# Performance work log

Hardware: AMD Instinct MI355X
Metric: run time of the kernel (lower is better)

Reference implementation:

```python
import jax, jax.numpy as jnp
import numpy as np

DIM = 768
HID = 3072
HID2 = HID // 2
MAX_LEVEL = 8
N_LEV = MAX_LEVEL + 1
BATCH, SEQ = 2, 2048
EPS = 1e-5


def _layernorm(x, gamma, beta):
    m = jnp.mean(x, axis=-1, keepdims=True)
    v = jnp.mean(jnp.square(x - m), axis=-1, keepdims=True)
    return (x - m) * jax.lax.rsqrt(v + EPS) * gamma + beta


def setup_inputs() -> dict:
    key = jax.random.key(0)
    ks = jax.random.split(key, 12)
    s = 0.02
    return {
        "x": jax.random.normal(ks[0], (BATCH, SEQ, DIM), dtype=jnp.float32),
        "levels_info": jax.random.randint(ks[1], (SEQ, 4), 0, N_LEV, dtype=jnp.int32),
        "gamma": jnp.ones((DIM,), dtype=jnp.float32),
        "beta": jnp.zeros((DIM,), dtype=jnp.float32),
        "W1": jax.random.normal(ks[2], (DIM, HID), dtype=jnp.float32) * s,
        "b1": jnp.zeros((HID,), dtype=jnp.float32),
        "W2": jax.random.normal(ks[3], (HID, DIM), dtype=jnp.float32) * s,
        "b2": jnp.zeros((DIM,), dtype=jnp.float32),
        "A1": jax.random.normal(ks[4], (N_LEV, DIM, HID2), dtype=jnp.float32) * s,
        "a1b": jnp.zeros((N_LEV, HID2), dtype=jnp.float32),
        "A2": jax.random.normal(ks[5], (N_LEV, HID2, DIM), dtype=jnp.float32) * s,
        "a2b": jnp.zeros((N_LEV, DIM), dtype=jnp.float32),
        "lmw": jnp.ones((N_LEV,), dtype=jnp.float32)
        + jax.random.normal(ks[6], (N_LEV,), dtype=jnp.float32) * 0.1,
    }


def reference(x, levels_info, gamma, beta, W1, b1, W2, b2, A1, a1b, A2, a2b, lmw):
    # x: [B,S,D]
    x_norm = _layernorm(x, gamma, beta)
    # main MLP: Linear -> GELU (exact, torch default) -> Linear; dropout=0 is identity
    h = jax.nn.gelu(jnp.einsum("bsd,dh->bsh", x_norm, W1) + b1, approximate=False)
    main_out = jnp.einsum("bsh,hd->bsd", h, W2) + b2

    # per-token depth-indexed adapter routing
    depths = jnp.clip(levels_info[:, 0], 0, MAX_LEVEL)  # [S]
    level_adapted = jnp.zeros_like(main_out)
    for lvl in range(N_LEV):  # small fixed expert set
        mask = (depths == lvl).astype(x.dtype)[None, :, None]  # [1,S,1]
        hl = jax.nn.relu(jnp.einsum("bsd,dh->bsh", x_norm, A1[lvl]) + a1b[lvl])
        level_adapted = level_adapted + mask * (
            jnp.einsum("bsh,hd->bsd", hl, A2[lvl]) + a2b[lvl]
        )

    # softmax over the sequence axis (faithful to F.softmax(..., dim=0))
    mix = jax.nn.softmax(lmw[depths], axis=0)[None, :, None]  # [1,S,1]
    return main_out * (1.0 - mix) + level_adapted * mix
```

## Files before the change

kernel.cpp:

```cpp
#include <hip/hip_runtime.h>
#include <hip/hip_bf16.h>
#include <math.h>

typedef __bf16 bf16;
typedef __bf16 bf16x4 __attribute__((ext_vector_type(4)));
typedef __bf16 bf16x8 __attribute__((ext_vector_type(8)));
typedef float f32x4 __attribute__((ext_vector_type(4)));

#define DIM 768
#define HID 3072
#define HID2 1536
#define NLEV 9
#define SEQ 2048
#define ROWS 4096
#define MAXPAD 5248
#define MAXTILES 41

__device__ __forceinline__ void gld16(const void* g, void* l) {
    __builtin_amdgcn_global_load_lds(
        (const __attribute__((address_space(1))) void*)g,
        (__attribute__((address_space(3))) void*)l, 16, 0, 0);
}


__device__ __forceinline__ void ln_body(int row, float* sm,
                                        const float* __restrict__ x,
                                        const float* __restrict__ gamma,
                                        const float* __restrict__ beta,
                                        bf16* __restrict__ xn) {
    int tid = threadIdx.x;
    const float* xr = x + (size_t)row * DIM;
    float v0 = xr[tid], v1 = xr[tid + 256], v2 = xr[tid + 512];
    float s = v0 + v1 + v2;
    float q = v0 * v0 + v1 * v1 + v2 * v2;
    for (int off = 32; off; off >>= 1) {
        s += __shfl_down(s, off, 64);
        q += __shfl_down(q, off, 64);
    }
    int wv = tid >> 6, ln = tid & 63;
    if (ln == 0) { sm[wv] = s; sm[4 + wv] = q; }
    __syncthreads();
    if (tid == 0) {
        float S = sm[0] + sm[1] + sm[2] + sm[3];
        float Q = sm[4] + sm[5] + sm[6] + sm[7];
        float m = S * (1.0f / DIM);
        float var = Q * (1.0f / DIM) - m * m;
        sm[8] = m;
        sm[9] = rsqrtf(var + 1e-5f);
    }
    __syncthreads();
    float m = sm[8], r = sm[9];
    bf16* xo = xn + (size_t)row * DIM;
    xo[tid]       = (bf16)((v0 - m) * r * gamma[tid]       + beta[tid]);
    xo[tid + 256] = (bf16)((v1 - m) * r * gamma[tid + 256] + beta[tid + 256]);
    xo[tid + 512] = (bf16)((v2 - m) * r * gamma[tid + 512] + beta[tid + 512]);
}

__device__ __forceinline__ void transpose_body(float* sm,
                                               const float* __restrict__ inb,
                                               bf16* __restrict__ outb,
                                               int R, int C, int bx, int by) {
    float (*tile)[33] = (float (*)[33])sm;
    int tx = threadIdx.x & 31, ty = threadIdx.x >> 5;
#pragma unroll
    for (int i = 0; i < 4; i++) {
        int r = by * 32 + ty + i * 8;
        tile[ty + i * 8][tx] = inb[(size_t)r * C + bx * 32 + tx];
    }
    __syncthreads();
#pragma unroll
    for (int i = 0; i < 4; i++) {
        int c = bx * 32 + ty + i * 8;
        outb[(size_t)c * R + by * 32 + tx] = (bf16)tile[tx][ty + i * 8];
    }
}

__device__ __forceinline__ void routing_body(float* sm,
                                             const int* __restrict__ levels_info,
                                             const float* __restrict__ lmw,
                                             float* __restrict__ mix,
                                             int* __restrict__ row_index,
                                             int* __restrict__ tile_meta,
                                             float* __restrict__ zbuf) {
    int* cnt = (int*)sm;
    int* cur = cnt + NLEV;
    int* off = cur + NLEV;
    float* mixv = (float*)(off + NLEV);
    int tid = threadIdx.x;
    if (tid < NLEV) { cnt[tid] = 0; cur[tid] = 0; }
    __syncthreads();
    for (int s = tid; s < SEQ; s += 256) {
        int d = levels_info[s * 4];
        d = d < 0 ? 0 : (d > 8 ? 8 : d);
        atomicAdd(&cnt[d], 1);
    }
    for (int i = tid; i < MAXPAD; i += 256) row_index[i] = -1;
    if (tid < 16) zbuf[tid] = 0.0f;
    __syncthreads();
    if (tid == 0) {
        float mx = lmw[0];
        for (int l = 1; l < NLEV; l++) mx = fmaxf(mx, lmw[l]);
        float denom = 0.f;
        for (int l = 0; l < NLEV; l++) denom += (float)cnt[l] * expf(lmw[l] - mx);
        float inv = 1.0f / denom;
        int running = 0, t = 0;
        for (int l = 0; l < NLEV; l++) {
            mixv[l] = expf(lmw[l] - mx) * inv;
            off[l] = running;
            int seg = (2 * cnt[l] + 127) & ~127;
            for (int k = 0; k < seg / 128; k++) tile_meta[t++] = l;
            running += seg;
        }
        for (; t < MAXTILES; t++) tile_meta[t] = -1;
    }
    __syncthreads();
    for (int s = tid; s < SEQ; s += 256) {
        int d = levels_info[s * 4];
        d = d < 0 ? 0 : (d > 8 ? 8 : d);
        int p = atomicAdd(&cur[d], 2);
        row_index[off[d] + p]     = s;
        row_index[off[d] + p + 1] = s + SEQ;
        mix[s] = mixv[d];
    }
}

__global__ __launch_bounds__(256) void prep_kernel(const float* __restrict__ x,
                                                   const int* __restrict__ levels_info,
                                                   const float* __restrict__ gamma,
                                                   const float* __restrict__ beta,
                                                   const float* __restrict__ W1,
                                                   const float* __restrict__ W2,
                                                   const float* __restrict__ A1,
                                                   const float* __restrict__ A2,
                                                   const float* __restrict__ lmw,
                                                   bf16* __restrict__ Xn,
                                                   bf16* __restrict__ W1t,
                                                   bf16* __restrict__ W2t,
                                                   bf16* __restrict__ A1t,
                                                   bf16* __restrict__ A2t,
                                                   float* __restrict__ mix,
                                                   int* __restrict__ row_index,
                                                   int* __restrict__ tile_meta,
                                                   float* __restrict__ zbuf) {
    __shared__ __align__(16) float sm[32 * 33];
    int bid = blockIdx.x;
    if (bid == 0) { routing_body(sm, levels_info, lmw, mix, row_index, tile_meta, zbuf); return; }
    bid -= 1;
    if (bid < ROWS) { ln_body(bid, sm, x, gamma, beta, Xn); return; }
    bid -= ROWS;
    if (bid < 2304) {
        transpose_body(sm, W1, W1t, DIM, HID, bid % 96, bid / 96);
        return;
    }
    bid -= 2304;
    if (bid < 2304) {
        transpose_body(sm, W2, W2t, HID, DIM, bid % 24, bid / 24);
        return;
    }
    bid -= 2304;
    if (bid < 10368) {
        int bz = bid / 1152, r = bid % 1152;
        transpose_body(sm, A1 + (size_t)bz * DIM * HID2, A1t + (size_t)bz * DIM * HID2,
                       DIM, HID2, r % 48, r / 48);
        return;
    }
    bid -= 10368;
    {
        int bz = bid / 1152, r = bid % 1152;
        transpose_body(sm, A2 + (size_t)bz * HID2 * DIM, A2t + (size_t)bz * HID2 * DIM,
                       HID2, DIM, r % 24, r / 24);
    }
}

__device__ __forceinline__ void gemm_loop_db(const bf16* ga0, const bf16* ga1,
                                             int stepa0, int stepa1,
                                             const bf16* gb0, const bf16* gb1, int stepb,
                                             bf16* As, bf16* Bs,
                                             f32x4 (&acc)[4][4], int ktiles) {
    int tid = threadIdx.x;
    int wv = tid >> 6;
    int lane = tid & 63;
    int wm = wv >> 1, wn = wv & 1;
    int aoff = ((wm * 64) + (lane & 15)) * 32 + (lane >> 4) * 8;
    int boff = ((wn * 64) + (lane & 15)) * 32 + (lane >> 4) * 8;
    gld16(ga0, As + wv * 512);
    gld16(ga1, As + 2048 + wv * 512);
    gld16(gb0, Bs + wv * 512);
    gld16(gb1, Bs + 2048 + wv * 512);
    ga0 += stepa0; ga1 += stepa1; gb0 += stepb; gb1 += stepb;
    for (int kt = 0; kt < ktiles; ++kt) {
        __syncthreads();
        int cur = (kt & 1) << 12;
        int nxt = cur ^ 4096;
        if (kt + 1 < ktiles) {
            gld16(ga0, As + nxt + wv * 512);
            gld16(ga1, As + nxt + 2048 + wv * 512);
            gld16(gb0, Bs + nxt + wv * 512);
            gld16(gb1, Bs + nxt + 2048 + wv * 512);
            ga0 += stepa0; ga1 += stepa1; gb0 += stepb; gb1 += stepb;
        }
        bf16x8 af[4], bfr[4];
#pragma unroll
        for (int i = 0; i < 4; i++) af[i] = *(const bf16x8*)(As + cur + aoff + i * 512);
#pragma unroll
        for (int j = 0; j < 4; j++) bfr[j] = *(const bf16x8*)(Bs + cur + boff + j * 512);
#pragma unroll
        for (int i = 0; i < 4; i++)
#pragma unroll
            for (int j = 0; j < 4; j++)
                acc[i][j] = __builtin_amdgcn_mfma_f32_16x16x32_bf16(af[i], bfr[j], acc[i][j], 0, 0, 0);
    }
}

#define ACC_INIT(acc) \
    _Pragma("unroll") for (int i = 0; i < 4; i++) \
    _Pragma("unroll") for (int j = 0; j < 4; j++) acc[i][j] = (f32x4){0.f, 0.f, 0.f, 0.f};

__global__ __launch_bounds__(256) void mlp1_kernel(const bf16* __restrict__ Xn,
                                                   const bf16* __restrict__ W1t,
                                                   const float* __restrict__ b1,
                                                   bf16* __restrict__ H,
                                                   const bf16* __restrict__ A1t,
                                                   const float* __restrict__ a1b,
                                                   const int* __restrict__ row_index,
                                                   const int* __restrict__ tile_meta,
                                                   const bf16* __restrict__ zbuf,
                                                   bf16* __restrict__ HL) {
    __shared__ __align__(16) bf16 As[8192], Bs[8192];
    int bid = blockIdx.x, tid = threadIdx.x;
    int r0 = tid >> 2, cg = tid & 3;
    int lane = tid & 63, wv = tid >> 6, wm = wv >> 1, wn = wv & 1;
    f32x4 acc[4][4];
    ACC_INIT(acc);

    if (bid < 768) {
        int mb = bid & 31, nb = bid >> 5;
        const bf16* ga0 = Xn + (size_t)(mb * 128 + r0) * DIM + cg * 8;
        const bf16* ga1 = ga0 + (size_t)64 * DIM;
        const bf16* gb0 = W1t + (size_t)(nb * 128 + r0) * DIM + cg * 8;
        const bf16* gb1 = gb0 + (size_t)64 * DIM;
        gemm_loop_db(ga0, ga1, 32, 32, gb0, gb1, 32, As, Bs, acc, DIM / 32);
        int rbase = mb * 128 + wm * 64 + ((lane >> 4) << 2);
        int cbase = nb * 128 + wn * 64 + (lane & 15);
#pragma unroll
        for (int j = 0; j < 4; j++) {
            int c = cbase + j * 16;
            float bias = b1[c];
#pragma unroll
            for (int i = 0; i < 4; i++)
#pragma unroll
                for (int r = 0; r < 4; r++) {
                    int row = rbase + i * 16 + r;
                    float v = acc[i][j][r] + bias;
                    float g = 0.5f * v * (1.0f + erff(v * 0.70710678118f));
                    H[(size_t)row * HID + c] = (bf16)g;
                }
        }
    } else {
        int t2 = bid - 768;
        int t = t2 % MAXTILES, nb = t2 / MAXTILES;
        int lvl = tile_meta[t];
        if (lvl < 0) return;
        int ridx0 = row_index[t * 128 + r0];
        int ridx1 = row_index[t * 128 + 64 + r0];
        const bf16* ga0 = (ridx0 >= 0) ? (Xn + (size_t)ridx0 * DIM + cg * 8) : zbuf;
        const bf16* ga1 = (ridx1 >= 0) ? (Xn + (size_t)ridx1 * DIM + cg * 8) : zbuf;
        int sa0 = (ridx0 >= 0) ? 32 : 0;
        int sa1 = (ridx1 >= 0) ? 32 : 0;
        const bf16* Bl = A1t + (size_t)lvl * HID2 * DIM;
        const bf16* gb0 = Bl + (size_t)(nb * 128 + r0) * DIM + cg * 8;
        const bf16* gb1 = gb0 + (size_t)64 * DIM;
        gemm_loop_db(ga0, ga1, sa0, sa1, gb0, gb1, 32, As, Bs, acc, DIM / 32);
        int rbase = wm * 64 + ((lane >> 4) << 2);
        int cbase = nb * 128 + wn * 64 + (lane & 15);
#pragma unroll
        for (int j = 0; j < 4; j++) {
            int c = cbase + j * 16;
            float bias = a1b[lvl * HID2 + c];
#pragma unroll
            for (int i = 0; i < 4; i++)
#pragma unroll
                for (int r = 0; r < 4; r++) {
                    int rl = rbase + i * 16 + r;
                    float v = acc[i][j][r] + bias;
                    HL[(size_t)(t * 128 + rl) * HID2 + c] = (bf16)fmaxf(v, 0.0f);
                }
        }
    }
}

__global__ __launch_bounds__(256) void mlp2_kernel(const bf16* __restrict__ H,
                                                   const bf16* __restrict__ W2t,
                                                   bf16* __restrict__ part,
                                                   const bf16* __restrict__ HL,
                                                   const bf16* __restrict__ A2t,
                                                   const float* __restrict__ a2b,
                                                   const int* __restrict__ row_index,
                                                   const int* __restrict__ tile_meta,
                                                   bf16* __restrict__ apart) {
    __shared__ __align__(16) bf16 As[8192], Bs[8192];
    int bid = blockIdx.x, tid = threadIdx.x;
    int r0 = tid >> 2, cg = tid & 3;
    int lane = tid & 63, wv = tid >> 6, wm = wv >> 1, wn = wv & 1;
    f32x4 acc[4][4];
    ACC_INIT(acc);

    if (bid < 384) {
        int mb = bid & 31;
        int rest = bid >> 5;
        int nb = rest % 6;
        int ks = rest / 6;
        const bf16* ga0 = H + (size_t)(mb * 128 + r0) * HID + ks * 1536 + cg * 8;
        const bf16* ga1 = ga0 + (size_t)64 * HID;
        const bf16* gb0 = W2t + (size_t)(nb * 128 + r0) * HID + ks * 1536 + cg * 8;
        const bf16* gb1 = gb0 + (size_t)64 * HID;
        gemm_loop_db(ga0, ga1, 32, 32, gb0, gb1, 32, As, Bs, acc, 48);
        bf16* pk = part + (size_t)ks * ROWS * DIM;
        int rbase = mb * 128 + wm * 64 + ((lane >> 4) << 2);
        int cbase = nb * 128 + wn * 64 + (lane & 15);
#pragma unroll
        for (int j = 0; j < 4; j++) {
            int c = cbase + j * 16;
#pragma unroll
            for (int i = 0; i < 4; i++)
#pragma unroll
                for (int r = 0; r < 4; r++) {
                    int row = rbase + i * 16 + r;
                    pk[(size_t)row * DIM + c] = (bf16)acc[i][j][r];
                }
        }
    } else {
        int t2 = bid - 384;
        int t = t2 % MAXTILES, nb = t2 / MAXTILES;
        int lvl = tile_meta[t];
        if (lvl < 0) return;
        const bf16* ga0 = HL + (size_t)(t * 128 + r0) * HID2 + cg * 8;
        const bf16* ga1 = ga0 + (size_t)64 * HID2;
        const bf16* Bl = A2t + (size_t)lvl * DIM * HID2;
        const bf16* gb0 = Bl + (size_t)(nb * 128 + r0) * HID2 + cg * 8;
        const bf16* gb1 = gb0 + (size_t)64 * HID2;
        gemm_loop_db(ga0, ga1, 32, 32, gb0, gb1, 32, As, Bs, acc, HID2 / 32);
        int rbase = wm * 64 + ((lane >> 4) << 2);
        int cbase = nb * 128 + wn * 64 + (lane & 15);
#pragma unroll
        for (int i = 0; i < 4; i++)
#pragma unroll
            for (int r = 0; r < 4; r++) {
                int rl = rbase + i * 16 + r;
                int rg = row_index[t * 128 + rl];
                if (rg >= 0) {
#pragma unroll
                    for (int j = 0; j < 4; j++) {
                        int c = cbase + j * 16;
                        apart[(size_t)rg * DIM + c] = (bf16)(acc[i][j][r] + a2b[lvl * DIM + c]);
                    }
                }
            }
    }
}

__global__ __launch_bounds__(256) void combine_kernel(const bf16* __restrict__ part,
                                                      const bf16* __restrict__ apart,
                                                      const float* __restrict__ b2,
                                                      const float* __restrict__ mix,
                                                      float* __restrict__ out) {
    int i = blockIdx.x * 256 + threadIdx.x;
    int base = i * 4;
    int row = base / DIM;
    int c = base - row * DIM;
    float mx = mix[row & (SEQ - 1)];
    bf16x4 p0 = *(const bf16x4*)(part + base);
    bf16x4 p1 = *(const bf16x4*)(part + (size_t)ROWS * DIM + base);
    bf16x4 ap = *(const bf16x4*)(apart + base);
    float4 o;
    float* po = &o.x;
#pragma unroll
    for (int k = 0; k < 4; k++) {
        float main_v = (float)p0[k] + (float)p1[k] + b2[c + k];
        po[k] = (1.0f - mx) * main_v + mx * (float)ap[k];
    }
    *(float4*)(out + base) = o;
}

extern "C" void kernel_launch(void* const* d_in, const int* in_sizes, int n_in,
                              void* d_out, int out_size, void* d_ws, size_t ws_size,
                              hipStream_t stream) {
    const float* x    = (const float*)d_in[0];
    const int* levels = (const int*)d_in[1];
    const float* gamma= (const float*)d_in[2];
    const float* beta = (const float*)d_in[3];
    const float* W1   = (const float*)d_in[4];
    const float* b1   = (const float*)d_in[5];
    const float* W2   = (const float*)d_in[6];
    const float* b2   = (const float*)d_in[7];
    const float* A1   = (const float*)d_in[8];
    const float* a1b  = (const float*)d_in[9];
    const float* A2   = (const float*)d_in[10];
    const float* a2b  = (const float*)d_in[11];
    const float* lmw  = (const float*)d_in[12];
    float* out = (float*)d_out;

    char* p = (char*)d_ws;
    auto alloc = [&](size_t bytes) {
        char* r = p;
        p += (bytes + 255) & ~(size_t)255;
        return r;
    };
    bf16* Xn   = (bf16*)alloc((size_t)ROWS * DIM * 2);
    bf16* W1t  = (bf16*)alloc((size_t)HID * DIM * 2);
    bf16* W2t  = (bf16*)alloc((size_t)DIM * HID * 2);
    bf16* A1t  = (bf16*)alloc((size_t)NLEV * HID2 * DIM * 2);
    bf16* A2t  = (bf16*)alloc((size_t)NLEV * DIM * HID2 * 2);
    bf16* H    = (bf16*)alloc((size_t)ROWS * HID * 2);
    bf16* HL   = (bf16*)alloc((size_t)MAXPAD * HID2 * 2);
    bf16* part = (bf16*)alloc((size_t)2 * ROWS * DIM * 2);
    bf16* apart= (bf16*)alloc((size_t)ROWS * DIM * 2);
    float* mix = (float*)alloc(SEQ * 4);
    int* row_index = (int*)alloc(MAXPAD * 4);
    int* tile_meta = (int*)alloc(MAXTILES * 4);
    float* zbuf    = (float*)alloc(64);

    prep_kernel<<<dim3(1 + ROWS + 2304 + 2304 + 10368 + 10368), dim3(256), 0, stream>>>(
        x, levels, gamma, beta, W1, W2, A1, A2, lmw,
        Xn, W1t, W2t, A1t, A2t, mix, row_index, tile_meta, zbuf);

    mlp1_kernel<<<dim3(768 + MAXTILES * 12), dim3(256), 0, stream>>>(
        Xn, W1t, b1, H, A1t, a1b, row_index, tile_meta, (const bf16*)zbuf, HL);

    mlp2_kernel<<<dim3(384 + MAXTILES * 6), dim3(256), 0, stream>>>(
        H, W2t, part, HL, A2t, a2b, row_index, tile_meta, apart);

    combine_kernel<<<dim3(ROWS * DIM / 1024), dim3(256), 0, stream>>>(
        part, apart, b2, mix, out);
}
```

Baseline: 295.9 us.

## Use 64x64 vectorized weight transposes and XOR-swizzle GEMM LDS tiles

Replaces the 32x32 scalar fp32→bf16 transpose with a 64x64 tile that loads float4 and stores 16-byte bf16x8 vectors, cutting the prep block count by four and widening memory transactions. Separately, the GEMM shared-memory tiles get an XOR swizzle: the global→LDS chunk index (cg) and the MFMA fragment read offset are permuted consistently to reduce LDS bank conflicts on the 16-byte fragment loads. The larger transpose tile raises LDS use in prep blocks, which can lower occupancy. The swizzle must match exactly between writes and reads, or results are silently wrong.

```diff
diff --git a/kernel.cpp b/kernel.cpp
--- a/kernel.cpp
+++ b/kernel.cpp
@@ -56,22 +56,33 @@
     xo[tid + 512] = (bf16)((v2 - m) * r * gamma[tid + 512] + beta[tid + 512]);
 }
 
-__device__ __forceinline__ void transpose_body(float* sm,
-                                               const float* __restrict__ inb,
-                                               bf16* __restrict__ outb,
-                                               int R, int C, int bx, int by) {
-    float (*tile)[33] = (float (*)[33])sm;
-    int tx = threadIdx.x & 31, ty = threadIdx.x >> 5;
-#pragma unroll
-    for (int i = 0; i < 4; i++) {
-        int r = by * 32 + ty + i * 8;
-        tile[ty + i * 8][tx] = inb[(size_t)r * C + bx * 32 + tx];
-    }
-    __syncthreads();
-#pragma unroll
-    for (int i = 0; i < 4; i++) {
-        int c = bx * 32 + ty + i * 8;
-        outb[(size_t)c * R + by * 32 + tx] = (bf16)tile[tx][ty + i * 8];
+__device__ __forceinline__ void transpose_body64(float* sm,
+                                                 const float* __restrict__ inb,
+                                                 bf16* __restrict__ outb,
+                                                 int R, int C, int bx, int by) {
+    int tid = threadIdx.x;
+    int ty = tid >> 4;
+    int tx4 = (tid & 15) * 4;
+#pragma unroll
+    for (int p = 0; p < 4; p++) {
+        int rloc = p * 16 + ty;
+        int row = by * 64 + rloc;
+        float4 v = *(const float4*)(inb + (size_t)row * C + bx * 64 + tx4);
+        sm[rloc * 65 + tx4 + 0] = v.x;
+        sm[rloc * 65 + tx4 + 1] = v.y;
+        sm[rloc * 65 + tx4 + 2] = v.z;
+        sm[rloc * 65 + tx4 + 3] = v.w;
+    }
+    __syncthreads();
+    int ch = tid & 7;
+    int ocb = tid >> 3;
+#pragma unroll
+    for (int p = 0; p < 2; p++) {
+        int oc = p * 32 + ocb;
+        bf16x8 tmp;
+#pragma unroll
+        for (int k = 0; k < 8; k++) tmp[k] = (bf16)sm[(ch * 8 + k) * 65 + oc];
+        *(bf16x8*)(outb + (size_t)(bx * 64 + oc) * R + by * 64 + ch * 8) = tmp;
     }
 }
 
@@ -142,33 +153,33 @@
                                                    int* __restrict__ row_index,
                                                    int* __restrict__ tile_meta,
                                                    float* __restrict__ zbuf) {
-    __shared__ __align__(16) float sm[32 * 33];
+    __shared__ __align__(16) float sm[64 * 65];
     int bid = blockIdx.x;
     if (bid == 0) { routing_body(sm, levels_info, lmw, mix, row_index, tile_meta, zbuf); return; }
     bid -= 1;
     if (bid < ROWS) { ln_body(bid, sm, x, gamma, beta, Xn); return; }
     bid -= ROWS;
-    if (bid < 2304) {
-        transpose_body(sm, W1, W1t, DIM, HID, bid % 96, bid / 96);
+    if (bid < 576) {
+        transpose_body64(sm, W1, W1t, DIM, HID, bid % 48, bid / 48);
         return;
     }
-    bid -= 2304;
-    if (bid < 2304) {
-        transpose_body(sm, W2, W2t, HID, DIM, bid % 24, bid / 24);
+    bid -= 576;
+    if (bid < 576) {
+        transpose_body64(sm, W2, W2t, HID, DIM, bid % 12, bid / 12);
         return;
     }
-    bid -= 2304;
-    if (bid < 10368) {
-        int bz = bid / 1152, r = bid % 1152;
-        transpose_body(sm, A1 + (size_t)bz * DIM * HID2, A1t + (size_t)bz * DIM * HID2,
-                       DIM, HID2, r % 48, r / 48);
+    bid -= 576;
+    if (bid < 2592) {
+        int bz = bid / 288, r = bid % 288;
+        transpose_body64(sm, A1 + (size_t)bz * DIM * HID2, A1t + (size_t)bz * DIM * HID2,
+                         DIM, HID2, r % 24, r / 24);
         return;
     }
-    bid -= 10368;
+    bid -= 2592;
     {
-        int bz = bid / 1152, r = bid % 1152;
-        transpose_body(sm, A2 + (size_t)bz * HID2 * DIM, A2t + (size_t)bz * HID2 * DIM,
-                       HID2, DIM, r % 24, r / 24);
+        int bz = bid / 288, r = bid % 288;
+        transpose_body64(sm, A2 + (size_t)bz * HID2 * DIM, A2t + (size_t)bz * HID2 * DIM,
+                         HID2, DIM, r % 12, r / 12);
     }
 }
 
@@ -181,8 +192,10 @@
     int wv = tid >> 6;
     int lane = tid & 63;
     int wm = wv >> 1, wn = wv & 1;
-    int aoff = ((wm * 64) + (lane & 15)) * 32 + (lane >> 4) * 8;
-    int boff = ((wn * 64) + (lane & 15)) * 32 + (lane >> 4) * 8;
+    int swz = (lane >> 1) & 3;
+    int achunk = ((lane >> 4) ^ swz) * 8;
+    int aoff = ((wm * 64) + (lane & 15)) * 32 + achunk;
+    int boff = ((wn * 64) + (lane & 15)) * 32 + achunk;
     gld16(ga0, As + wv * 512);
     gld16(ga1, As + 2048 + wv * 512);
     gld16(gb0, Bs + wv * 512);
@@ -216,6 +229,8 @@
     _Pragma("unroll") for (int i = 0; i < 4; i++) \
     _Pragma("unroll") for (int j = 0; j < 4; j++) acc[i][j] = (f32x4){0.f, 0.f, 0.f, 0.f};
 
+#define SWZ_CG(tid) (((tid) & 3) ^ (((tid) >> 3) & 3))
+
 __global__ __launch_bounds__(256) void mlp1_kernel(const bf16* __restrict__ Xn,
                                                    const bf16* __restrict__ W1t,
                                                    const float* __restrict__ b1,
@@ -228,7 +243,7 @@
                                                    bf16* __restrict__ HL) {
     __shared__ __align__(16) bf16 As[8192], Bs[8192];
     int bid = blockIdx.x, tid = threadIdx.x;
-    int r0 = tid >> 2, cg = tid & 3;
+    int r0 = tid >> 2, cg = SWZ_CG(tid);
     int lane = tid & 63, wv = tid >> 6, wm = wv >> 1, wn = wv & 1;
     f32x4 acc[4][4];
     ACC_INIT(acc);
@@ -300,7 +315,7 @@
                                                    bf16* __restrict__ apart) {
     __shared__ __align__(16) bf16 As[8192], Bs[8192];
     int bid = blockIdx.x, tid = threadIdx.x;
-    int r0 = tid >> 2, cg = tid & 3;
+    int r0 = tid >> 2, cg = SWZ_CG(tid);
     int lane = tid & 63, wv = tid >> 6, wm = wv >> 1, wn = wv & 1;
     f32x4 acc[4][4];
     ACC_INIT(acc);
@@ -420,7 +435,7 @@
     int* tile_meta = (int*)alloc(MAXTILES * 4);
     float* zbuf    = (float*)alloc(64);
 
-    prep_kernel<<<dim3(1 + ROWS + 2304 + 2304 + 10368 + 10368), dim3(256), 0, stream>>>(
+    prep_kernel<<<dim3(1 + ROWS + 576 + 576 + 2592 + 2592), dim3(256), 0, stream>>>(
         x, levels, gamma, beta, W1, W2, A1, A2, lmw,
         Xn, W1t, W2t, A1t, A2t, mix, row_index, tile_meta, zbuf);
 
```

After: 292.5 us. No clear change (-1.1%).
